# Kernel tuning notes

Hardware: AMD Instinct MI355X
Metric: run time of the kernel (lower is better)

Reference implementation:

```python
import jax, jax.numpy as jnp
import numpy as np

B, N, D, H = 4, 2048, 768, 12
HD = D // H  # head_dim = 64


def setup_inputs() -> dict:
    key = jax.random.key(0)
    k1, k2, k3 = jax.random.split(key, 3)
    z = jax.random.normal(k1, (B, N, D), dtype=jnp.float32)
    # per-head qkv Linear weights, torch Linear convention: y = x @ W.T + b
    Wqkv = jax.random.normal(k2, (H, 3 * HD, D), dtype=jnp.float32) * 0.02
    bqkv = jnp.zeros((H, 3 * HD), dtype=jnp.float32)
    Wmsa = jax.random.normal(k3, (D, D), dtype=jnp.float32) * 0.02
    bmsa = jnp.zeros((D,), dtype=jnp.float32)
    return {"z": z, "Wqkv": Wqkv, "bqkv": bqkv, "Wmsa": Wmsa, "bmsa": bmsa}


def reference(z, Wqkv, bqkv, Wmsa, bmsa):
    # All heads' qkv projections in one einsum: [B,N,D] x [H,3hd,D] -> [B,H,N,3hd]
    qkv = jnp.einsum("bnd,hed->bhne", z, Wqkv) + bqkv[None, :, None, :]
    q, k, v = jnp.split(qkv, 3, axis=-1)  # each [B,H,N,hd]
    scale = 1.0 / jnp.sqrt(jnp.asarray(HD, dtype=z.dtype))
    scores = jnp.einsum("bhqd,bhkd->bhqk", q, k) * scale  # [B,H,N,N]
    attn = jax.nn.softmax(scores, axis=-1)
    out = jnp.einsum("bhqk,bhkd->bhqd", attn, v)  # [B,H,N,hd]
    # concat heads (head order matches the torch per-head cat)
    out = out.transpose(0, 2, 1, 3).reshape(B, N, H * HD)  # [B,N,D]
    return out @ Wmsa.T + bmsa
```

## Files before the change

### kernel.cpp

```cpp
#include <hip/hip_runtime.h>

typedef unsigned short u16;
typedef unsigned int u32;
typedef __attribute__((ext_vector_type(8))) short bf16x8;
typedef __attribute__((ext_vector_type(4))) float f32x4;

#define B_ 4
#define H_ 12
#define N_ 2048
#define D_ 768
#define HD_ 64
#define NTOK (B_ * N_)
#define NE   (H_ * 3 * HD_)

#define BK 64
#define CPITCH 144

#define QSCALE 0.18033688011112042f

__device__ __forceinline__ u16 f2bf(float f) {
    u32 u = __float_as_uint(f);
    u += 0x7fffu + ((u >> 16) & 1u);
    return (u16)(u >> 16);
}

__device__ __forceinline__ f32x4 mfma16(bf16x8 a, bf16x8 b, f32x4 c) {
    return __builtin_amdgcn_mfma_f32_16x16x32_bf16(a, b, c, 0, 0, 0);
}

__device__ __forceinline__ void g2l16(const u16* g, u16* l) {
    __builtin_amdgcn_global_load_lds(
        (const __attribute__((address_space(1))) void*)g,
        (__attribute__((address_space(3))) void*)l, 16, 0, 0);
}

#define NZ4  (NTOK * D_ / 4)
#define NWQ4 (NE * D_ / 4)
#define NWM4 (D_ * D_ / 4)
__global__ __launch_bounds__(256) void cvt_all(const float* __restrict__ z,
                                               const float* __restrict__ Wq,
                                               const float* __restrict__ Wm,
                                               u16* __restrict__ Xbf,
                                               u16* __restrict__ Wqb,
                                               u16* __restrict__ Wmb) {
    int i = blockIdx.x * blockDim.x + threadIdx.x;
    const float* src;
    u16* dst;
    int j;
    if (i < NZ4) {
        src = z; dst = Xbf; j = i;
    } else if (i < NZ4 + NWQ4) {
        src = Wq; dst = Wqb; j = i - NZ4;
    } else if (i < NZ4 + NWQ4 + NWM4) {
        src = Wm; dst = Wmb; j = i - NZ4 - NWQ4;
    } else {
        return;
    }
    float4 v = ((const float4*)src)[j];
    u32 lo = (u32)f2bf(v.x) | ((u32)f2bf(v.y) << 16);
    u32 hi = (u32)f2bf(v.z) | ((u32)f2bf(v.w) << 16);
    ((uint2*)dst)[j] = make_uint2(lo, hi);
}

#define GEMM_CORE(Xp, Wp, TM, SMELEMS)                                         \
    __shared__ u16 smem[SMELEMS];                                              \
    u16* ldsA = smem;                                          \
    u16* ldsB = smem + 2 * (TM) * BK;                         \
    const int tid = threadIdx.x;                                               \
    const int wave = tid >> 6, lane = tid & 63;                                \
    const int lrow = lane & 15, quad = lane >> 4;                              \
    const int flat_ = blockIdx.x;                                              \
    const int mbase = (((flat_ & 7) << 4) | ((flat_ >> 3) & 15)) * (TM);       \
    const int nbase = (flat_ >> 7) * 128;                                      \
    const int srow = tid >> 3;                                      \
    const int schunk = tid & 7;                                                \
    const int sk = (schunk ^ (srow & 7)) << 3;   \
    const int sdst = srow * BK + schunk * 8;     \
    const u16* gA = Xp + (size_t)(mbase + srow) * D_ + sk;                     \
    const u16* gB = Wp + (size_t)(nbase + srow) * D_ + sk;                     \
    const int m_ofs = (wave >> 1) * ((TM) / 2);                                \
    const int n_ofs = (wave & 1) * 64;                                         \
    const int e_ = lrow & 7;                                                   \
    const int offA0 = (m_ofs + lrow) * BK + ((quad ^ e_) << 3);                \
    const int offB0 = (n_ofs + lrow) * BK + ((quad ^ e_) << 3);                \
    f32x4 acc[(TM) / 32][4] = {};                                              \
    _Pragma("unroll") for (int i = 0; i < (TM) / 32; i++)                      \
        g2l16(gA + (size_t)(32 * i) * D_, ldsA + sdst + i * 32 * BK);          \
    _Pragma("unroll") for (int i = 0; i < 4; i++)                              \
        g2l16(gB + (size_t)(32 * i) * D_, ldsB + sdst + i * 32 * BK);          \
    for (int it = 0; it < D_ / BK; it++) {                                     \
        const int cur = it & 1;                                                \
        const int abase = cur * (TM) * BK, bbase = cur * 128 * BK;             \
        __syncthreads();   \
        if (it + 1 < D_ / BK) {                                                \
            const int kt2 = (it + 1) * BK;                                     \
            const int nb = cur ^ 1;                                            \
            _Pragma("unroll") for (int i = 0; i < (TM) / 32; i++)              \
                g2l16(gA + (size_t)(32 * i) * D_ + kt2,                        \
                      ldsA + nb * (TM) * BK + sdst + i * 32 * BK);             \
            _Pragma("unroll") for (int i = 0; i < 4; i++)                      \
                g2l16(gB + (size_t)(32 * i) * D_ + kt2,                        \
                      ldsB + nb * 128 * BK + sdst + i * 32 * BK);              \
        }                                                                      \
        _Pragma("unroll") for (int ks = 0; ks < 2; ks++) {                     \
            const int oa = abase + (offA0 ^ (ks << 5));                       \
            const int ob = bbase + (offB0 ^ (ks << 5));                       \
            bf16x8 af[(TM) / 32], bfr[4];                                      \
            _Pragma("unroll") for (int c = 0; c < (TM) / 32; c++)              \
                af[c] = *(const bf16x8*)&ldsA[oa + c * 16 * BK];               \
            _Pragma("unroll") for (int c = 0; c < 4; c++)                      \
                bfr[c] = *(const bf16x8*)&ldsB[ob + c * 16 * BK];              \
            _Pragma("unroll") for (int i = 0; i < (TM) / 32; i++)              \
                _Pragma("unroll") for (int j = 0; j < 4; j++)                  \
                    acc[i][j] = mfma16(af[i], bfr[j], acc[i][j]);              \
        }                                                                      \
    }

__global__ __launch_bounds__(256) void gemm_qkv(const u16* __restrict__ X,
                                                const u16* __restrict__ W,
                                                const float* __restrict__ bqkv,
                                                u16* __restrict__ Qs,
                                                u16* __restrict__ Ks,
                                                u16* __restrict__ Vt) {
    GEMM_CORE(X, W, 64, 24576)
    __syncthreads();
    u16* ldsC = smem;
#pragma unroll
    for (int cn = 0; cn < 4; cn++) {
        const int E = nbase + n_ofs + cn * 16;
        const int h = E / 192;
        const int rr = E - h * 192;
        const int kind = rr >> 6;
        const float bias = bqkv[E + lrow];
        if (kind == 2) {
            const int d = (rr & 63) + lrow;
#pragma unroll
            for (int cm = 0; cm < 2; cm++) {
                const int t0 = mbase + m_ofs + cm * 16 + quad * 4;
                const int b_ = t0 >> 11, n0 = t0 & (N_ - 1);
                const size_t bh = (size_t)(b_ * H_ + h);
                uint2 pk;
                pk.x = (u32)f2bf(acc[cm][cn][0] + bias) |
                       ((u32)f2bf(acc[cm][cn][1] + bias) << 16);
                pk.y = (u32)f2bf(acc[cm][cn][2] + bias) |
                       ((u32)f2bf(acc[cm][cn][3] + bias) << 16);
                *(uint2*)&Vt[(bh * HD_ + d) * N_ + n0] = pk;
            }
        } else {
            const int fcol = n_ofs + cn * 16 + lrow;
            const float scale = (kind == 0) ? QSCALE : 1.0f;
#pragma unroll
            for (int cm = 0; cm < 2; cm++)
#pragma unroll
                for (int r = 0; r < 4; r++) {
                    const int tok = m_ofs + cm * 16 + quad * 4 + r;
                    ldsC[tok * CPITCH + fcol] =
                        f2bf((acc[cm][cn][r] + bias) * scale);
                }
        }
    }
    __syncthreads();
    {
        const int tok = tid >> 2, sub = tid & 3;
        const int fh = sub >> 1, jh = sub & 1;
        const int gf = nbase + fh * 64;
        const int kind2 = (gf >> 6) % 3;
        if (kind2 != 2) {
            const int h2 = gf / 192;
            const int t = mbase + tok;
            const int b2 = t >> 11, n2 = t & (N_ - 1);
            u16* dst = (kind2 == 0 ? Qs : Ks) +
                       ((size_t)(b2 * H_ + h2) * N_ + n2) * HD_;
            const u16* src = &ldsC[tok * CPITCH + fh * 64];
#pragma unroll
            for (int j = 0; j < 4; j++)
                *(uint4*)&dst[(jh * 4 + j) * 8] =
                    *(const uint4*)&src[(jh * 4 + j) * 8];
        }
    }
}

__global__ __launch_bounds__(256) void gemm_out(const u16* __restrict__ X2,
                                                const u16* __restrict__ W,
                                                const float* __restrict__ bmsa,
                                                float* __restrict__ out) {
    GEMM_CORE(X2, W, 64, 24576)
#pragma unroll
    for (int cn = 0; cn < 4; cn++) {
        const int col = nbase + n_ofs + cn * 16 + lrow;
        const float bias = bmsa[col];
#pragma unroll
        for (int cm = 0; cm < 2; cm++) {
#pragma unroll
            for (int r = 0; r < 4; r++) {
                const int t = mbase + m_ofs + cm * 16 + quad * 4 + r;
                out[(size_t)t * D_ + col] = acc[cm][cn][r] + bias;
            }
        }
    }
}

__global__ __launch_bounds__(256, 3) void flash_attn(const u16* __restrict__ Qs,
                                                     const u16* __restrict__ Ks,
                                                     const u16* __restrict__ Vt,
                                                     u16* __restrict__ X2) {
    __shared__ u16 ldsK[2][64 * HD_];
    __shared__ u16 ldsV[2][64 * HD_];
    __shared__ u16 ldsP[4][2][16][68];
    const int tid = threadIdx.x;
    const int wave = tid >> 6, lane = tid & 63;
    const int lrow = lane & 15, quad = lane >> 4;
    const int x_ = blockIdx.x;
    const int j_ = x_ >> 3;
    const int bh = (x_ & 7) * 6 + (j_ >> 4);
    const int qb = j_ & 15;
    const int qbase = qb * 128 + wave * 32;
    const int b = bh / H_, h = bh - b * H_;

    const u16* Kb = Ks + (size_t)bh * N_ * HD_;
    const u16* Vb = Vt + (size_t)bh * HD_ * N_;

    const int srow = tid >> 3;
    const int schunk = tid & 7;
    const int skk = (schunk ^ (srow & 7)) << 3;
    const int sdst = srow * HD_ + schunk * 8;

    bf16x8 qa[2][2];
#pragma unroll
    for (int t = 0; t < 2; t++) {
        const u16* Qb = Qs + ((size_t)bh * N_ + qbase + t * 16 + lrow) * HD_ + quad * 8;
        qa[t][0] = *(const bf16x8*)(Qb);
        qa[t][1] = *(const bf16x8*)(Qb + 32);
    }

    const int fofs = (quad ^ (lrow & 7)) << 3;
    const short onebf = (short)0x3F80;
    const bf16x8 ones = {onebf, onebf, onebf, onebf, onebf, onebf, onebf, onebf};

    f32x4 Oacc[2][4] = {};
    f32x4 lacc[2] = {};

    {
        const u16* gK = Kb + (size_t)srow * HD_ + skk;
        g2l16(gK, &ldsK[0][sdst]);
        g2l16(gK + (size_t)32 * HD_, &ldsK[0][sdst + 32 * HD_]);
        const u16* gV = Vb + (size_t)srow * N_ + skk;
        g2l16(gV, &ldsV[0][sdst]);
        g2l16(gV + (size_t)32 * N_, &ldsV[0][sdst + 32 * HD_]);
    }

    for (int it = 0; it < N_ / 64; it++) {
        const int cur = it & 1;
        __syncthreads();
        if (it + 1 < N_ / 64) {
            const int kt2 = (it + 1) << 6;
            const u16* gK = Kb + (size_t)(kt2 + srow) * HD_ + skk;
            g2l16(gK, &ldsK[cur ^ 1][sdst]);
            g2l16(gK + (size_t)32 * HD_, &ldsK[cur ^ 1][sdst + 32 * HD_]);
            const u16* gV = Vb + (size_t)srow * N_ + kt2 + skk;
            g2l16(gV, &ldsV[cur ^ 1][sdst]);
            g2l16(gV + (size_t)32 * N_, &ldsV[cur ^ 1][sdst + 32 * HD_]);
        }
        bf16x8 kf[8];
#pragma unroll
        for (int c = 0; c < 4; c++) {
            const int o = (c * 16 + lrow) * HD_ + fofs;
            kf[2 * c]     = *(const bf16x8*)&ldsK[cur][o];
            kf[2 * c + 1] = *(const bf16x8*)&ldsK[cur][o ^ 32];
        }
        f32x4 s[2][4] = {};
        __builtin_amdgcn_s_setprio(1);
#pragma unroll
        for (int t = 0; t < 2; t++)
#pragma unroll
            for (int c = 0; c < 4; c++) {
                s[t][c] = mfma16(kf[2 * c], qa[t][0], s[t][c]);
                s[t][c] = mfma16(kf[2 * c + 1], qa[t][1], s[t][c]);
            }
        __builtin_amdgcn_s_setprio(0);
#pragma unroll
        for (int t = 0; t < 2; t++)
#pragma unroll
            for (int c = 0; c < 4; c++) {
                u32 b0 = __float_as_uint(__builtin_amdgcn_exp2f(s[t][c][0]));
                u32 b1 = __float_as_uint(__builtin_amdgcn_exp2f(s[t][c][1]));
                u32 b2 = __float_as_uint(__builtin_amdgcn_exp2f(s[t][c][2]));
                u32 b3 = __float_as_uint(__builtin_amdgcn_exp2f(s[t][c][3]));
                uint2 pk;
                pk.x = __builtin_amdgcn_perm(b1, b0, 0x07060302u);
                pk.y = __builtin_amdgcn_perm(b3, b2, 0x07060302u);
                *(uint2*)&ldsP[wave][t][lrow][c * 16 + quad * 4] = pk;
            }
        bf16x8 pa[2][2];
#pragma unroll
        for (int t = 0; t < 2; t++) {
            pa[t][0] = *(const bf16x8*)&ldsP[wave][t][lrow][quad * 8];
            pa[t][1] = *(const bf16x8*)&ldsP[wave][t][lrow][32 + quad * 8];
        }
        __builtin_amdgcn_s_setprio(1);
#pragma unroll
        for (int t = 0; t < 2; t++) {
            lacc[t] = mfma16(pa[t][0], ones, lacc[t]);
            lacc[t] = mfma16(pa[t][1], ones, lacc[t]);
        }
#pragma unroll
        for (int c = 0; c < 4; c++) {
            const int o = (c * 16 + lrow) * HD_ + fofs;
            bf16x8 v0 = *(const bf16x8*)&ldsV[cur][o];
            bf16x8 v1 = *(const bf16x8*)&ldsV[cur][o ^ 32];
#pragma unroll
            for (int t = 0; t < 2; t++) {
                Oacc[t][c] = mfma16(pa[t][0], v0, Oacc[t][c]);
                Oacc[t][c] = mfma16(pa[t][1], v1, Oacc[t][c]);
            }
        }
        __builtin_amdgcn_s_setprio(0);
    }
#pragma unroll
    for (int t = 0; t < 2; t++)
#pragma unroll
        for (int r = 0; r < 4; r++) {
            const float inv = 1.0f / lacc[t][r];
            const int qrow = qbase + t * 16 + quad * 4 + r;
#pragma unroll
            for (int c = 0; c < 4; c++) {
                X2[((size_t)b * N_ + qrow) * D_ + h * HD_ + c * 16 + lrow] =
                    f2bf(Oacc[t][c][r] * inv);
            }
        }
}

extern "C" void kernel_launch(void* const* d_in, const int* in_sizes, int n_in,
                              void* d_out, int out_size, void* d_ws, size_t ws_size,
                              hipStream_t stream) {
    const float* z    = (const float*)d_in[0];
    const float* Wqkv = (const float*)d_in[1];
    const float* bqkv = (const float*)d_in[2];
    const float* Wmsa = (const float*)d_in[3];
    const float* bmsa = (const float*)d_in[4];
    float* out = (float*)d_out;

    u16* Xbf = (u16*)d_ws;
    u16* Wqb = Xbf + (size_t)NTOK * D_;
    u16* Wmb = Wqb + (size_t)NE * D_;
    u16* Qs  = Wmb + (size_t)D_ * D_;
    u16* Ks  = Qs + (size_t)B_ * H_ * N_ * HD_;
    u16* Vt  = Ks + (size_t)B_ * H_ * N_ * HD_;
    u16* X2  = Vt + (size_t)B_ * H_ * N_ * HD_;

    const int ntot = NZ4 + NWQ4 + NWM4;
    cvt_all<<<(ntot + 255) / 256, 256, 0, stream>>>(z, Wqkv, Wmsa, Xbf, Wqb, Wmb);

    gemm_qkv<<<dim3((NTOK / 64) * (NE / 128)), 256, 0, stream>>>(Xbf, Wqb, bqkv, Qs, Ks, Vt);
    flash_attn<<<dim3(768), 256, 0, stream>>>(Qs, Ks, Vt, X2);
    gemm_out<<<dim3((NTOK / 64) * (D_ / 128)), 256, 0, stream>>>(X2, Wmb, bmsa, out);
}
```

Before: 200.4 us.

## Load K/V fragments directly from global memory instead of LDS staging

Removes the double-buffered LDS staging of K and V tiles, along with the per-iteration __syncthreads, and has each wave load its MFMA fragments straight from global memory (through L2/L1). This drops the block barrier and the LDS traffic and frees LDS for occupancy. In exchange, each of the four waves now fetches the same K/V data separately, the loads are no longer prefetched one tile ahead, and global-load latency sits on the critical path of every iteration.

```diff
diff --git a/kernel.cpp b/kernel.cpp
--- a/kernel.cpp
+++ b/kernel.cpp
@@ -204,8 +204,6 @@
                                                      const u16* __restrict__ Ks,
                                                      const u16* __restrict__ Vt,
                                                      u16* __restrict__ X2) {
-    __shared__ u16 ldsK[2][64 * HD_];
-    __shared__ u16 ldsV[2][64 * HD_];
     __shared__ u16 ldsP[4][2][16][68];
     const int tid = threadIdx.x;
     const int wave = tid >> 6, lane = tid & 63;
@@ -219,11 +217,8 @@
 
     const u16* Kb = Ks + (size_t)bh * N_ * HD_;
     const u16* Vb = Vt + (size_t)bh * HD_ * N_;
-
-    const int srow = tid >> 3;
-    const int schunk = tid & 7;
-    const int skk = (schunk ^ (srow & 7)) << 3;
-    const int sdst = srow * HD_ + schunk * 8;
+    const u16* Kl = Kb + (size_t)lrow * HD_ + quad * 8;
+    const u16* Vl = Vb + (size_t)lrow * N_ + quad * 8;
 
     bf16x8 qa[2][2];
 #pragma unroll
@@ -233,40 +228,20 @@
         qa[t][1] = *(const bf16x8*)(Qb + 32);
     }
 
-    const int fofs = (quad ^ (lrow & 7)) << 3;
     const short onebf = (short)0x3F80;
     const bf16x8 ones = {onebf, onebf, onebf, onebf, onebf, onebf, onebf, onebf};
 
     f32x4 Oacc[2][4] = {};
     f32x4 lacc[2] = {};
 
-    {
-        const u16* gK = Kb + (size_t)srow * HD_ + skk;
-        g2l16(gK, &ldsK[0][sdst]);
-        g2l16(gK + (size_t)32 * HD_, &ldsK[0][sdst + 32 * HD_]);
-        const u16* gV = Vb + (size_t)srow * N_ + skk;
-        g2l16(gV, &ldsV[0][sdst]);
-        g2l16(gV + (size_t)32 * N_, &ldsV[0][sdst + 32 * HD_]);
-    }
-
     for (int it = 0; it < N_ / 64; it++) {
-        const int cur = it & 1;
-        __syncthreads();
-        if (it + 1 < N_ / 64) {
-            const int kt2 = (it + 1) << 6;
-            const u16* gK = Kb + (size_t)(kt2 + srow) * HD_ + skk;
-            g2l16(gK, &ldsK[cur ^ 1][sdst]);
-            g2l16(gK + (size_t)32 * HD_, &ldsK[cur ^ 1][sdst + 32 * HD_]);
-            const u16* gV = Vb + (size_t)srow * N_ + kt2 + skk;
-            g2l16(gV, &ldsV[cur ^ 1][sdst]);
-            g2l16(gV + (size_t)32 * N_, &ldsV[cur ^ 1][sdst + 32 * HD_]);
-        }
+        const int kt = it << 6;
         bf16x8 kf[8];
 #pragma unroll
         for (int c = 0; c < 4; c++) {
-            const int o = (c * 16 + lrow) * HD_ + fofs;
-            kf[2 * c]     = *(const bf16x8*)&ldsK[cur][o];
-            kf[2 * c + 1] = *(const bf16x8*)&ldsK[cur][o ^ 32];
+            const u16* kp = Kl + (size_t)(kt + c * 16) * HD_;
+            kf[2 * c]     = *(const bf16x8*)(kp);
+            kf[2 * c + 1] = *(const bf16x8*)(kp + 32);
         }
         f32x4 s[2][4] = {};
         __builtin_amdgcn_s_setprio(1);
@@ -278,6 +253,13 @@
                 s[t][c] = mfma16(kf[2 * c + 1], qa[t][1], s[t][c]);
             }
         __builtin_amdgcn_s_setprio(0);
+        bf16x8 vf[8];
+#pragma unroll
+        for (int c = 0; c < 4; c++) {
+            const u16* vp = Vl + (size_t)(c * 16) * N_ + kt;
+            vf[2 * c]     = *(const bf16x8*)(vp);
+            vf[2 * c + 1] = *(const bf16x8*)(vp + 32);
+        }
 #pragma unroll
         for (int t = 0; t < 2; t++)
 #pragma unroll
@@ -305,13 +287,10 @@
         }
 #pragma unroll
         for (int c = 0; c < 4; c++) {
-            const int o = (c * 16 + lrow) * HD_ + fofs;
-            bf16x8 v0 = *(const bf16x8*)&ldsV[cur][o];
-            bf16x8 v1 = *(const bf16x8*)&ldsV[cur][o ^ 32];
 #pragma unroll
             for (int t = 0; t < 2; t++) {
-                Oacc[t][c] = mfma16(pa[t][0], v0, Oacc[t][c]);
-                Oacc[t][c] = mfma16(pa[t][1], v1, Oacc[t][c]);
+                Oacc[t][c] = mfma16(pa[t][0], vf[2 * c], Oacc[t][c]);
+                Oacc[t][c] = mfma16(pa[t][1], vf[2 * c + 1], Oacc[t][c]);
             }
         }
         __builtin_amdgcn_s_setprio(0);
```

After: 312.0 us. 55.7% more time.
